# Performance work log

Measured on AMD Instinct MI355X. Metric: run time of the kernel, lower is better.

The kernel has to match this reference:

```python
import jax, jax.numpy as jnp
import numpy as np

B, L, S, V, I, H = 4096, 16, 512, 512, 512, 512  # batch, attn_length, attn_size, attn_vec_size, input_size, lstm hidden


def setup_inputs() -> dict:
    key = jax.random.key(0)
    ks = jax.random.split(key, 16)
    rn = lambda k, sh, sc=1.0: jax.random.normal(k, sh, dtype=jnp.float32) * sc
    return {
        "inputs": rn(ks[0], (B, I)),
        "cell_c": rn(ks[1], (B, H)),
        "cell_h": rn(ks[2], (B, H)),
        "attns": rn(ks[3], (B, S)),
        "attn_states": rn(ks[4], (B, L, S)),
        "W1": rn(ks[5], (I + S, I), 0.02),
        "b1": jnp.zeros((I,), jnp.float32),
        "Wx": rn(ks[6], (I, 4 * H), 0.02),
        "Wh": rn(ks[7], (H, 4 * H), 0.02),
        "b_lstm": jnp.zeros((4 * H,), jnp.float32),
        "W3": rn(ks[8], (2 * H, V), 0.02),
        "b3": jnp.zeros((V,), jnp.float32),
        "k": rn(ks[9], (1, 1, S, V), 0.02),
        "v": rn(ks[10], (1, 1, S, V), 0.02),
        "W2": rn(ks[11], (H + S, S), 0.02),
        "b2": jnp.zeros((S,), jnp.float32),
    }


def reference(inputs, cell_c, cell_h, attns, attn_states, W1, b1, Wx, Wh, b_lstm, W3, b3, k, v, W2, b2):
    # linear1: project [inputs; attns] -> cell input
    x = jnp.concatenate([inputs, attns], axis=1) @ W1 + b1  # [B, I]
    # LSTM cell step (gate order i, f, g, o)
    gates = x @ Wx + cell_h @ Wh + b_lstm  # [B, 4H]
    i, f, g, o = jnp.split(gates, 4, axis=1)
    c_new = jax.nn.sigmoid(f) * cell_c + jax.nn.sigmoid(i) * jnp.tanh(g)
    h_new = jax.nn.sigmoid(o) * jnp.tanh(c_new)
    # attention over attn_states with query = concat(new_state)
    query = jnp.concatenate([c_new, h_new], axis=1)  # [B, 2H]
    # 1x1 conv over [B, L, 1, S] with kernel [1,1,S,V] == matmul over S
    hf = jnp.einsum('bls,sv->blv', attn_states, k[0, 0])  # [B, L, V]
    y = query @ W3 + b3  # [B, V]
    t = jnp.tanh(hf + y[:, None, :])  # [B, L, V]
    # reduce_sum(v * t, [2,3]) with v [1,1,S,V] broadcast against t [B,L,1,V]
    # == einsum over V with v summed over its S axis (t independent of S axis)
    vsum = v[0, 0].sum(axis=0)  # [V]
    s = jnp.einsum('blv,v->bl', t, vsum)  # [B, L]
    a = jax.nn.softmax(s, axis=1)
    d = jnp.einsum('bl,bls->bs', a, attn_states)  # new_attns [B, S]
    # output projection on [cell_output; new_attns]
    output = jnp.concatenate([h_new, d], axis=1) @ W2 + b2  # [B, S]
    # shift attention window: drop oldest, append output
    new_attn_states = jnp.concatenate([attn_states[:, 1:, :], output[:, None, :]], axis=1)
    new_attn_states = new_attn_states.reshape(inputs.shape[0], L * S)
    return output, c_new, h_new, d, new_attn_states
```

## Files before the change

### kernel.cpp

```cpp
#include <hip/hip_runtime.h>
#include <hip/hip_bf16.h>
#include <math.h>

#define BB 4096
#define LL 16
#define SS 512
#define VV 512
#define II 512
#define HH 512

typedef __attribute__((ext_vector_type(4))) float f32x4;
typedef __attribute__((ext_vector_type(8))) short short8;

#define GLOBAL_AS __attribute__((address_space(1)))
#define LDS_AS __attribute__((address_space(3)))

__device__ __forceinline__ unsigned short f2bf(float f) {
    union { float f; unsigned u; } c; c.f = f;
    unsigned u = c.u + 0x7FFFu + ((c.u >> 16) & 1u);
    return (unsigned short)(u >> 16);
}
__device__ __forceinline__ float bf2f(unsigned short u) {
    union { unsigned u; float f; } c; c.u = ((unsigned)u) << 16;
    return c.f;
}
__device__ __forceinline__ float fast_tanh(float x) {
    return 1.f - 2.f / (__expf(2.f * x) + 1.f);
}

template<int MODE, int NF>
__global__ __launch_bounds__(256) void gemm_mfma(
    const ushort* __restrict__ A, const ushort* __restrict__ Bt,
    const float* __restrict__ bias, void* __restrict__ C, float* __restrict__ C2,
    int ldc, int M, int N, int K) {
    constexpr int BN = NF * 32;
    __shared__ ushort Als[128 * 64];
    __shared__ ushort Bls[BN * 64];
    const int tid  = threadIdx.x;
    const int lane = tid & 63;
    const int w    = tid >> 6;
    const int wm   = w >> 1, wn = w & 1;
    const int brow = blockIdx.y * 128;
    const int bcol = blockIdx.x * BN;
    f32x4 acc[4][NF] = {};
    const int nkt = K >> 6;
    for (int kt = 0; kt < nkt; ++kt) {
        __syncthreads();
        #pragma unroll
        for (int i = 0; i < 4; ++i) {
            int c0 = i * 256 + w * 64;
            int c  = c0 + lane;
            int row = c >> 3, sl = c & 7;
            const ushort* gp = A + (size_t)(brow + row) * K + kt * 64 + ((sl ^ (row & 7)) * 8);
            __builtin_amdgcn_global_load_lds((const GLOBAL_AS void*)gp,
                                             (LDS_AS void*)(Als + c0 * 8), 16, 0, 0);
        }
        #pragma unroll
        for (int i = 0; i < NF; ++i) {
            int c0 = i * 256 + w * 64;
            int c  = c0 + lane;
            int row = c >> 3, sl = c & 7;
            const ushort* gp = Bt + (size_t)(bcol + row) * K + kt * 64 + ((sl ^ (row & 7)) * 8);
            __builtin_amdgcn_global_load_lds((const GLOBAL_AS void*)gp,
                                             (LDS_AS void*)(Bls + c0 * 8), 16, 0, 0);
        }
        __syncthreads();
        const char* AlsB = (const char*)Als;
        const char* BlsB = (const char*)Bls;
        #pragma unroll
        for (int kh = 0; kh < 2; ++kh) {
            int ks = kh * 4 + (lane >> 4);
            short8 a[4], b[NF];
            #pragma unroll
            for (int m = 0; m < 4; ++m) {
                int row = wm * 64 + m * 16 + (lane & 15);
                a[m] = *(const short8*)(AlsB + (row * 8 + (ks ^ (row & 7))) * 16);
            }
            #pragma unroll
            for (int n = 0; n < NF; ++n) {
                int row = wn * (NF * 16) + n * 16 + (lane & 15);
                b[n] = *(const short8*)(BlsB + (row * 8 + (ks ^ (row & 7))) * 16);
            }
            #pragma unroll
            for (int m = 0; m < 4; ++m)
                #pragma unroll
                for (int n = 0; n < NF; ++n)
                    acc[m][n] = __builtin_amdgcn_mfma_f32_16x16x32_bf16(a[m], b[n], acc[m][n], 0, 0, 0);
        }
    }
    #pragma unroll
    for (int m = 0; m < 4; ++m)
        #pragma unroll
        for (int n = 0; n < NF; ++n)
            #pragma unroll
            for (int r = 0; r < 4; ++r) {
                int gm = brow + wm * 64 + m * 16 + (lane >> 4) * 4 + r;
                int gc = bcol + wn * (NF * 16) + n * 16 + (lane & 15);
                float v = acc[m][n][r] + bias[gc];
                if (MODE == 1) ((ushort*)C)[(size_t)gm * ldc + gc] = f2bf(v);
                else           ((float*)C)[(size_t)gm * ldc + gc] = v;
                if (MODE == 2) C2[((size_t)gm * 16 + 15) * 512 + gc] = v;
            }
}

__global__ __launch_bounds__(512, 4) void score_all(
    const float* __restrict__ ASf, const ushort* __restrict__ Bt,
    const float* __restrict__ Y, const float* __restrict__ vsum,
    float* __restrict__ o_ns, float* __restrict__ o_d, ushort* __restrict__ A7) {
    __shared__ ushort Als[64 * 64];
    __shared__ ushort Bls[512 * 64];
    __shared__ float sred[8][64];
    __shared__ float s_lds[64];
    const int tid  = threadIdx.x;
    const int lane = tid & 63;
    const int w    = tid >> 6;
    const int l15  = lane & 15, l4 = lane >> 4;
    const int brow = blockIdx.x * 64;
    const int bg0  = brow >> 4;
    f32x4 acc[4][4] = {};
    for (int kt = 0; kt < 8; ++kt) {
        __syncthreads();
        {
            int chunk = tid;
            int row = chunk >> 3, slot = chunk & 7;
            int gslot = slot ^ (row & 7);
            const float* gp = ASf + (size_t)(brow + row) * 512 + kt * 64 + gslot * 8;
            float4 f0 = *(const float4*)gp;
            float4 f1 = *(const float4*)(gp + 4);
            short8 pk;
            pk[0] = (short)f2bf(f0.x); pk[1] = (short)f2bf(f0.y);
            pk[2] = (short)f2bf(f0.z); pk[3] = (short)f2bf(f0.w);
            pk[4] = (short)f2bf(f1.x); pk[5] = (short)f2bf(f1.y);
            pk[6] = (short)f2bf(f1.z); pk[7] = (short)f2bf(f1.w);
            *(short8*)((char*)Als + chunk * 16) = pk;
        }
        #pragma unroll
        for (int i = 0; i < 8; ++i) {
            int c0 = i * 512 + w * 64;
            int c  = c0 + lane;
            int row = c >> 3, sl = c & 7;
            const ushort* gp = Bt + (size_t)row * 512 + kt * 64 + ((sl ^ (row & 7)) * 8);
            __builtin_amdgcn_global_load_lds((const GLOBAL_AS void*)gp,
                                             (LDS_AS void*)(Bls + c0 * 8), 16, 0, 0);
        }
        __syncthreads();
        const char* AlsB = (const char*)Als;
        const char* BlsB = (const char*)Bls;
        #pragma unroll
        for (int kh = 0; kh < 2; ++kh) {
            int ks = kh * 4 + l4;
            short8 a[4], b[4];
            #pragma unroll
            for (int m = 0; m < 4; ++m) {
                int row = m * 16 + l15;
                a[m] = *(const short8*)(AlsB + (row * 8 + (ks ^ (row & 7))) * 16);
            }
            #pragma unroll
            for (int n = 0; n < 4; ++n) {
                int rowb = w * 64 + n * 16 + l15;
                b[n] = *(const short8*)(BlsB + (rowb * 8 + (ks ^ (rowb & 7))) * 16);
            }
            #pragma unroll
            for (int m = 0; m < 4; ++m)
                #pragma unroll
                for (int n = 0; n < 4; ++n)
                    acc[m][n] = __builtin_amdgcn_mfma_f32_16x16x32_bf16(a[m], b[n], acc[m][n], 0, 0, 0);
        }
    }
    float part[4][4] = {};
    #pragma unroll
    for (int m = 0; m < 4; ++m) {
        int yb = bg0 + m;
        #pragma unroll
        for (int n = 0; n < 4; ++n) {
            int gc = w * 64 + n * 16 + l15;
            float yv = Y[(size_t)yb * 512 + gc];
            float vs = vsum[gc];
            #pragma unroll
            for (int r = 0; r < 4; ++r)
                part[m][r] += fast_tanh(acc[m][n][r] + yv) * vs;
        }
    }
    #pragma unroll
    for (int m = 0; m < 4; ++m)
        #pragma unroll
        for (int r = 0; r < 4; ++r) {
            float v = part[m][r];
            v += __shfl_xor(v, 1); v += __shfl_xor(v, 2);
            v += __shfl_xor(v, 4); v += __shfl_xor(v, 8);
            if (l15 == 0) sred[w][m * 16 + l4 * 4 + r] = v;
        }
    __syncthreads();
    if (tid < 64) {
        float v = 0.f;
        #pragma unroll
        for (int q = 0; q < 8; ++q) v += sred[q][tid];
        s_lds[tid] = v;
    }
    __syncthreads();

    {
        const int bat = w >> 1;
        const int bg  = bg0 + bat;
        const int c   = (w & 1) * 256 + lane * 4;
        float mx = -1e30f;
        #pragma unroll
        for (int l = 0; l < LL; ++l) mx = fmaxf(mx, s_lds[bat * 16 + l]);
        float wgt[LL]; float sum = 0.f;
        #pragma unroll
        for (int l = 0; l < LL; ++l) { wgt[l] = __expf(s_lds[bat * 16 + l] - mx); sum += wgt[l]; }
        const float inv = 1.f / sum;
        float d0 = 0.f, d1 = 0.f, d2 = 0.f, d3 = 0.f;
        #pragma unroll
        for (int l = 0; l < LL; ++l) {
            float4 v = *(const float4*)(ASf + ((size_t)bg * 16 + l) * 512 + c);
            if (l >= 1)
                *(float4*)(o_ns + ((size_t)bg * 16 + l - 1) * 512 + c) = v;
            d0 += wgt[l] * v.x; d1 += wgt[l] * v.y;
            d2 += wgt[l] * v.z; d3 += wgt[l] * v.w;
        }
        d0 *= inv; d1 *= inv; d2 *= inv; d3 *= inv;
        float4 dv; dv.x = d0; dv.y = d1; dv.z = d2; dv.w = d3;
        *(float4*)(o_d + (size_t)bg * 512 + c) = dv;
        ushort4 uv; uv.x = f2bf(d0); uv.y = f2bf(d1); uv.z = f2bf(d2); uv.w = f2bf(d3);
        *(ushort4*)(A7 + (size_t)bg * 1024 + 512 + c) = uv;
    }
}

struct TrJob { const float* srcA; const float* srcB; int K0; ushort* dst; int N; int K; };
struct TrJobs { TrJob j[5]; };

__global__ void tr_cvt_all(TrJobs jobs) {
    TrJob jb = jobs.j[blockIdx.z];
    int bn = blockIdx.x, bk = blockIdx.y;
    if (bn * 32 >= jb.N || bk * 32 >= jb.K) return;
    __shared__ float tile[32][33];
    int tx = threadIdx.x, ty = threadIdx.y;
    #pragma unroll
    for (int j = 0; j < 4; ++j) {
        int k = bk * 32 + ty + j * 8;
        const float* s = (k < jb.K0) ? (jb.srcA + (size_t)k * jb.N)
                                     : (jb.srcB + (size_t)(k - jb.K0) * jb.N);
        tile[ty + j * 8][tx] = s[bn * 32 + tx];
    }
    __syncthreads();
    #pragma unroll
    for (int j = 0; j < 4; ++j) {
        int n = bn * 32 + ty + j * 8;
        jb.dst[(size_t)n * jb.K + bk * 32 + tx] = f2bf(tile[tx][ty + j * 8]);
    }
}

struct CvJobs { const float* src[3]; ushort* dst[3]; };
__global__ void cvt_all(CvJobs jobs) {
    const float* src = jobs.src[blockIdx.y];
    ushort* dst = jobs.dst[blockIdx.y];
    int idx = blockIdx.x * 256 + threadIdx.x;
    int i4 = idx & 127, row = idx >> 7;
    float4 v = *(const float4*)(src + (size_t)row * 512 + i4 * 4);
    ushort4 o; o.x = f2bf(v.x); o.y = f2bf(v.y); o.z = f2bf(v.z); o.w = f2bf(v.w);
    *(ushort4*)(dst + (size_t)row * 1024 + i4 * 4) = o;
}

__global__ void lstm_ew(const float4* __restrict__ g4, const float4* __restrict__ cc4,
                        float4* __restrict__ c4, float4* __restrict__ h4,
                        ushort* __restrict__ A4, ushort* __restrict__ A7) {
    int idx = blockIdx.x * 256 + threadIdx.x;
    int b = idx >> 7, q = idx & 127;
    const float4* g = g4 + (size_t)b * 512;
    float4 gi = g[q], gf = g[q + 128], gg = g[q + 256], go = g[q + 384];
    float4 cc = cc4[idx];
    float4 c, h;
    #pragma unroll
    for (int j = 0; j < 4; ++j) {
        float fi = ((const float*)&gi)[j], ff = ((const float*)&gf)[j];
        float fg = ((const float*)&gg)[j], fo = ((const float*)&go)[j];
        float si = 1.f / (1.f + __expf(-fi));
        float sf = 1.f / (1.f + __expf(-ff));
        float so = 1.f / (1.f + __expf(-fo));
        float cv = sf * ((const float*)&cc)[j] + si * tanhf(fg);
        ((float*)&c)[j] = cv;
        ((float*)&h)[j] = so * tanhf(cv);
    }
    c4[idx] = c; h4[idx] = h;
    ushort4 uc, uh;
    uc.x = f2bf(c.x); uc.y = f2bf(c.y); uc.z = f2bf(c.z); uc.w = f2bf(c.w);
    uh.x = f2bf(h.x); uh.y = f2bf(h.y); uh.z = f2bf(h.z); uh.w = f2bf(h.w);
    *(ushort4*)(A4 + (size_t)b * 1024 + q * 4) = uc;
    *(ushort4*)(A4 + (size_t)b * 1024 + 512 + q * 4) = uh;
    *(ushort4*)(A7 + (size_t)b * 1024 + q * 4) = uh;
}

__global__ void vsum_k(const float* __restrict__ Vm, float* __restrict__ out) {
    __shared__ float red[8][32];
    int tc = threadIdx.x & 31, ts = threadIdx.x >> 5;
    int v = blockIdx.x * 32 + tc;
    float acc = 0.f;
    for (int s = ts; s < SS; s += 8) acc += Vm[(size_t)s * VV + v];
    red[ts][tc] = acc;
    __syncthreads();
    if (ts == 0) {
        float t = 0.f;
        #pragma unroll
        for (int j = 0; j < 8; ++j) t += red[j][tc];
        out[v] = t;
    }
}

extern "C" void kernel_launch(void* const* d_in, const int* in_sizes, int n_in,
                              void* d_out, int out_size, void* d_ws, size_t ws_size,
                              hipStream_t stream) {
    const float* inputs      = (const float*)d_in[0];
    const float* cell_c      = (const float*)d_in[1];
    const float* cell_h      = (const float*)d_in[2];
    const float* attns       = (const float*)d_in[3];
    const float* attn_states = (const float*)d_in[4];
    const float* W1          = (const float*)d_in[5];
    const float* b1          = (const float*)d_in[6];
    const float* Wx          = (const float*)d_in[7];
    const float* Wh          = (const float*)d_in[8];
    const float* b_lstm      = (const float*)d_in[9];
    const float* W3          = (const float*)d_in[10];
    const float* b3          = (const float*)d_in[11];
    const float* kmat        = (const float*)d_in[12];
    const float* vmat        = (const float*)d_in[13];
    const float* W2          = (const float*)d_in[14];
    const float* b2          = (const float*)d_in[15];

    float* o_out = (float*)d_out;
    float* o_c   = o_out + (size_t)BB * HH;
    float* o_h   = o_c   + (size_t)BB * HH;
    float* o_d   = o_h   + (size_t)BB * HH;
    float* o_ns  = o_d   + (size_t)BB * SS;

    float* ws_gates = (float*)d_ws;
    float* ws_y     = ws_gates + (size_t)BB * 4 * HH;
    float* ws_vsum  = ws_y + (size_t)BB * VV;
    ushort* A1    = (ushort*)(ws_vsum + VV);
    ushort* A2    = A1 + (size_t)BB * 1024;
    ushort* A4    = A2 + (size_t)BB * 1024;
    ushort* A7    = A4 + (size_t)BB * 1024;
    ushort* W1t   = A7 + (size_t)BB * 1024;
    ushort* WxWht = W1t + (size_t)512 * 1024;
    ushort* W3t   = WxWht + (size_t)2048 * 1024;
    ushort* W2t   = W3t + (size_t)512 * 1024;
    ushort* kTt   = W2t + (size_t)512 * 1024;

    TrJobs tj;
    tj.j[0] = {W1, W1, 1024, W1t, 512, 1024};
    tj.j[1] = {Wx, Wh, 512, WxWht, 2048, 1024};
    tj.j[2] = {W3, W3, 1024, W3t, 512, 1024};
    tj.j[3] = {W2, W2, 1024, W2t, 512, 1024};
    tj.j[4] = {kmat, kmat, 512, kTt, 512, 512};
    tr_cvt_all<<<dim3(64, 32, 5), dim3(32, 8), 0, stream>>>(tj);
    CvJobs cj;
    cj.src[0] = inputs; cj.dst[0] = A1;
    cj.src[1] = attns;  cj.dst[1] = A1 + 512;
    cj.src[2] = cell_h; cj.dst[2] = A2 + 512;
    cvt_all<<<dim3(BB * 128 / 256, 3), 256, 0, stream>>>(cj);
    vsum_k<<<16, 256, 0, stream>>>(vmat, ws_vsum);

    gemm_mfma<1, 1><<<dim3(512 / 32, BB / 128), 256, 0, stream>>>(
        A1, W1t, b1, A2, nullptr, 1024, BB, 512, 1024);
    gemm_mfma<0, 4><<<dim3(2048 / 128, BB / 128), 256, 0, stream>>>(
        A2, WxWht, b_lstm, ws_gates, nullptr, 2048, BB, 2048, 1024);
    lstm_ew<<<BB * 128 / 256, 256, 0, stream>>>(
        (const float4*)ws_gates, (const float4*)cell_c,
        (float4*)o_c, (float4*)o_h, A4, A7);
    gemm_mfma<0, 1><<<dim3(512 / 32, BB / 128), 256, 0, stream>>>(
        A4, W3t, b3, ws_y, nullptr, 512, BB, 512, 1024);
    score_all<<<BB * LL / 64, 512, 0, stream>>>(
        attn_states, kTt, ws_y, ws_vsum, o_ns, o_d, A7);
    gemm_mfma<2, 1><<<dim3(512 / 32, BB / 128), 256, 0, stream>>>(
        A7, W2t, b2, o_out, o_ns, 512, BB, 512, 1024);
}
```

Baseline: 235.4 us.

## Fuse LSTM elementwise into gate GEMM and double-buffer score_all K loop

Adds a gate GEMM whose weight columns are permuted at transpose time so each tile holds matching i/f/g/o columns. The LSTM elementwise step then runs in the GEMM epilogue, removing the fp32 gates buffer write and read and one kernel launch. Separately, score_all now streams K in 32-wide steps with double-buffered per-wave B tiles and prefetched A registers, cutting its LDS footprint and overlapping loads with MFMA. The fused epilogue writes scalar, poorly coalesced stores, and the hand-written waitcnt counts must match the number of loads in flight to stay correct.

```diff
diff --git a/kernel.cpp b/kernel.cpp
--- a/kernel.cpp
+++ b/kernel.cpp
@@ -103,12 +103,89 @@
             }
 }
 
+__global__ __launch_bounds__(256) void gemm_gates(
+    const ushort* __restrict__ A, const ushort* __restrict__ Bt,
+    const float* __restrict__ bias, const float* __restrict__ cc,
+    float* __restrict__ o_c, float* __restrict__ o_h,
+    ushort* __restrict__ A4, ushort* __restrict__ A7) {
+    __shared__ ushort Als[128 * 64];
+    __shared__ ushort Bls[64 * 64];
+    const int tid = threadIdx.x, lane = tid & 63, w = tid >> 6;
+    const int l15 = lane & 15, l4 = lane >> 4;
+    const int brow = blockIdx.y * 128;
+    const int xb = blockIdx.x;
+    f32x4 acc[2][4] = {};
+    for (int kt = 0; kt < 16; ++kt) {
+        __syncthreads();
+        #pragma unroll
+        for (int i = 0; i < 4; ++i) {
+            int c0 = i * 256 + w * 64, c = c0 + lane;
+            int row = c >> 3, sl = c & 7;
+            const ushort* gp = A + (size_t)(brow + row) * 1024 + kt * 64 + ((sl ^ (row & 7)) * 8);
+            __builtin_amdgcn_global_load_lds((const GLOBAL_AS void*)gp,
+                                             (LDS_AS void*)(Als + c0 * 8), 16, 0, 0);
+        }
+        #pragma unroll
+        for (int i = 0; i < 2; ++i) {
+            int c0 = i * 256 + w * 64, c = c0 + lane;
+            int row = c >> 3, sl = c & 7;
+            const ushort* gp = Bt + (size_t)(xb * 64 + row) * 1024 + kt * 64 + ((sl ^ (row & 7)) * 8);
+            __builtin_amdgcn_global_load_lds((const GLOBAL_AS void*)gp,
+                                             (LDS_AS void*)(Bls + c0 * 8), 16, 0, 0);
+        }
+        __syncthreads();
+        const char* AlsB = (const char*)Als;
+        const char* BlsB = (const char*)Bls;
+        #pragma unroll
+        for (int kh = 0; kh < 2; ++kh) {
+            int ks = kh * 4 + l4;
+            short8 a[2], b[4];
+            #pragma unroll
+            for (int m = 0; m < 2; ++m) {
+                int row = w * 32 + m * 16 + l15;
+                a[m] = *(const short8*)(AlsB + (row * 8 + (ks ^ (row & 7))) * 16);
+            }
+            #pragma unroll
+            for (int n = 0; n < 4; ++n) {
+                int row = n * 16 + l15;
+                b[n] = *(const short8*)(BlsB + (row * 8 + (ks ^ (row & 7))) * 16);
+            }
+            #pragma unroll
+            for (int m = 0; m < 2; ++m)
+                #pragma unroll
+                for (int n = 0; n < 4; ++n)
+                    acc[m][n] = __builtin_amdgcn_mfma_f32_16x16x32_bf16(a[m], b[n], acc[m][n], 0, 0, 0);
+        }
+    }
+    const int h = xb * 16 + l15;
+    #pragma unroll
+    for (int m = 0; m < 2; ++m)
+        #pragma unroll
+        for (int r = 0; r < 4; ++r) {
+            int gm = brow + w * 32 + m * 16 + l4 * 4 + r;
+            float gi = acc[m][0][r] + bias[h];
+            float gf = acc[m][1][r] + bias[512 + h];
+            float gg = acc[m][2][r] + bias[1024 + h];
+            float go = acc[m][3][r] + bias[1536 + h];
+            float si = 1.f / (1.f + __expf(-gi));
+            float sf = 1.f / (1.f + __expf(-gf));
+            float so = 1.f / (1.f + __expf(-go));
+            float cv = sf * cc[(size_t)gm * 512 + h] + si * tanhf(gg);
+            float hn = so * tanhf(cv);
+            o_c[(size_t)gm * 512 + h] = cv;
+            o_h[(size_t)gm * 512 + h] = hn;
+            A4[(size_t)gm * 1024 + h] = f2bf(cv);
+            A4[(size_t)gm * 1024 + 512 + h] = f2bf(hn);
+            A7[(size_t)gm * 1024 + h] = f2bf(hn);
+        }
+}
+
 __global__ __launch_bounds__(512, 4) void score_all(
     const float* __restrict__ ASf, const ushort* __restrict__ Bt,
     const float* __restrict__ Y, const float* __restrict__ vsum,
     float* __restrict__ o_ns, float* __restrict__ o_d, ushort* __restrict__ A7) {
-    __shared__ ushort Als[64 * 64];
-    __shared__ ushort Bls[512 * 64];
+    __shared__ ushort Als[64 * 40];
+    __shared__ ushort Bls[8][2][2048];
     __shared__ float sred[8][64];
     __shared__ float s_lds[64];
     const int tid  = threadIdx.x;
@@ -117,56 +194,65 @@
     const int l15  = lane & 15, l4 = lane >> 4;
     const int brow = blockIdx.x * 64;
     const int bg0  = brow >> 4;
+    const int arow = tid >> 3, aq = tid & 7;
+    const float* agp = ASf + (size_t)(brow + arow) * 512 + aq * 4;
+    const char* AlsB = (const char*)Als;
     f32x4 acc[4][4] = {};
-    for (int kt = 0; kt < 8; ++kt) {
-        __syncthreads();
+
+    #pragma unroll
+    for (int i = 0; i < 4; ++i) {
+        int cl = i * 64 + lane;
+        int r = cl >> 2, sl = cl & 3;
+        const ushort* gp = Bt + (size_t)(w * 64 + r) * 512 + ((sl ^ ((r >> 1) & 3)) * 8);
+        __builtin_amdgcn_global_load_lds((const GLOBAL_AS void*)gp,
+            (LDS_AS void*)(&Bls[w][0][i * 512] + lane * 8), 16, 0, 0);
+    }
+    float4 af = *(const float4*)agp;
+
+    #pragma unroll
+    for (int kt = 0; kt < 16; ++kt) {
+        const int buf = kt & 1;
+        asm volatile("s_waitcnt lgkmcnt(0)" ::: "memory");
+        __builtin_amdgcn_s_barrier();
         {
-            int chunk = tid;
-            int row = chunk >> 3, slot = chunk & 7;
-            int gslot = slot ^ (row & 7);
-            const float* gp = ASf + (size_t)(brow + row) * 512 + kt * 64 + gslot * 8;
-            float4 f0 = *(const float4*)gp;
-            float4 f1 = *(const float4*)(gp + 4);
-            short8 pk;
-            pk[0] = (short)f2bf(f0.x); pk[1] = (short)f2bf(f0.y);
-            pk[2] = (short)f2bf(f0.z); pk[3] = (short)f2bf(f0.w);
-            pk[4] = (short)f2bf(f1.x); pk[5] = (short)f2bf(f1.y);
-            pk[6] = (short)f2bf(f1.z); pk[7] = (short)f2bf(f1.w);
-            *(short8*)((char*)Als + chunk * 16) = pk;
-        }
-        #pragma unroll
-        for (int i = 0; i < 8; ++i) {
-            int c0 = i * 512 + w * 64;
-            int c  = c0 + lane;
-            int row = c >> 3, sl = c & 7;
-            const ushort* gp = Bt + (size_t)row * 512 + kt * 64 + ((sl ^ (row & 7)) * 8);
-            __builtin_amdgcn_global_load_lds((const GLOBAL_AS void*)gp,
-                                             (LDS_AS void*)(Bls + c0 * 8), 16, 0, 0);
-        }
-        __syncthreads();
-        const char* AlsB = (const char*)Als;
-        const char* BlsB = (const char*)Bls;
-        #pragma unroll
-        for (int kh = 0; kh < 2; ++kh) {
-            int ks = kh * 4 + l4;
-            short8 a[4], b[4];
-            #pragma unroll
-            for (int m = 0; m < 4; ++m) {
-                int row = m * 16 + l15;
-                a[m] = *(const short8*)(AlsB + (row * 8 + (ks ^ (row & 7))) * 16);
-            }
-            #pragma unroll
-            for (int n = 0; n < 4; ++n) {
-                int rowb = w * 64 + n * 16 + l15;
-                b[n] = *(const short8*)(BlsB + (rowb * 8 + (ks ^ (rowb & 7))) * 16);
-            }
-            #pragma unroll
-            for (int m = 0; m < 4; ++m)
-                #pragma unroll
-                for (int n = 0; n < 4; ++n)
-                    acc[m][n] = __builtin_amdgcn_mfma_f32_16x16x32_bf16(a[m], b[n], acc[m][n], 0, 0, 0);
-        }
-    }
+            ushort4 u; u.x = f2bf(af.x); u.y = f2bf(af.y); u.z = f2bf(af.z); u.w = f2bf(af.w);
+            *(ushort4*)((char*)Als + arow * 80 + aq * 8) = u;
+        }
+        if (kt < 15) {
+            #pragma unroll
+            for (int i = 0; i < 4; ++i) {
+                int cl = i * 64 + lane;
+                int r = cl >> 2, sl = cl & 3;
+                const ushort* gp = Bt + (size_t)(w * 64 + r) * 512 + (kt + 1) * 32
+                                   + ((sl ^ ((r >> 1) & 3)) * 8);
+                __builtin_amdgcn_global_load_lds((const GLOBAL_AS void*)gp,
+                    (LDS_AS void*)(&Bls[w][buf ^ 1][i * 512] + lane * 8), 16, 0, 0);
+            }
+            af = *(const float4*)(agp + (kt + 1) * 32);
+        }
+        asm volatile("s_waitcnt lgkmcnt(0)" ::: "memory");
+        __builtin_amdgcn_s_barrier();
+        if (kt < 15) asm volatile("s_waitcnt vmcnt(5)" ::: "memory");
+        else         asm volatile("s_waitcnt vmcnt(0)" ::: "memory");
+        short8 a[4], b[4];
+        #pragma unroll
+        for (int m = 0; m < 4; ++m) {
+            int row = m * 16 + l15;
+            a[m] = *(const short8*)(AlsB + row * 80 + l4 * 16);
+        }
+        #pragma unroll
+        for (int n = 0; n < 4; ++n) {
+            int r = n * 16 + l15;
+            int sl = l4 ^ ((r >> 1) & 3);
+            b[n] = *(const short8*)((const char*)&Bls[w][buf][0] + r * 64 + sl * 16);
+        }
+        #pragma unroll
+        for (int m = 0; m < 4; ++m)
+            #pragma unroll
+            for (int n = 0; n < 4; ++n)
+                acc[m][n] = __builtin_amdgcn_mfma_f32_16x16x32_bf16(a[m], b[n], acc[m][n], 0, 0, 0);
+    }
+
     float part[4][4] = {};
     #pragma unroll
     for (int m = 0; m < 4; ++m) {
@@ -227,7 +313,7 @@
     }
 }
 
-struct TrJob { const float* srcA; const float* srcB; int K0; ushort* dst; int N; int K; };
+struct TrJob { const float* srcA; const float* srcB; int K0; ushort* dst; int N; int K; int perm; };
 struct TrJobs { TrJob j[5]; };
 
 __global__ void tr_cvt_all(TrJobs jobs) {
@@ -247,7 +333,12 @@
     #pragma unroll
     for (int j = 0; j < 4; ++j) {
         int n = bn * 32 + ty + j * 8;
-        jb.dst[(size_t)n * jb.K + bk * 32 + tx] = f2bf(tile[tx][ty + j * 8]);
+        int nd = n;
+        if (jb.perm) {
+            int g = n >> 9, u = n & 511;
+            nd = (u >> 4) * 64 + g * 16 + (u & 15);
+        }
+        jb.dst[(size_t)nd * jb.K + bk * 32 + tx] = f2bf(tile[tx][ty + j * 8]);
     }
 }
 
@@ -260,35 +351,6 @@
     float4 v = *(const float4*)(src + (size_t)row * 512 + i4 * 4);
     ushort4 o; o.x = f2bf(v.x); o.y = f2bf(v.y); o.z = f2bf(v.z); o.w = f2bf(v.w);
     *(ushort4*)(dst + (size_t)row * 1024 + i4 * 4) = o;
-}
-
-__global__ void lstm_ew(const float4* __restrict__ g4, const float4* __restrict__ cc4,
-                        float4* __restrict__ c4, float4* __restrict__ h4,
-                        ushort* __restrict__ A4, ushort* __restrict__ A7) {
-    int idx = blockIdx.x * 256 + threadIdx.x;
-    int b = idx >> 7, q = idx & 127;
-    const float4* g = g4 + (size_t)b * 512;
-    float4 gi = g[q], gf = g[q + 128], gg = g[q + 256], go = g[q + 384];
-    float4 cc = cc4[idx];
-    float4 c, h;
-    #pragma unroll
-    for (int j = 0; j < 4; ++j) {
-        float fi = ((const float*)&gi)[j], ff = ((const float*)&gf)[j];
-        float fg = ((const float*)&gg)[j], fo = ((const float*)&go)[j];
-        float si = 1.f / (1.f + __expf(-fi));
-        float sf = 1.f / (1.f + __expf(-ff));
-        float so = 1.f / (1.f + __expf(-fo));
-        float cv = sf * ((const float*)&cc)[j] + si * tanhf(fg);
-        ((float*)&c)[j] = cv;
-        ((float*)&h)[j] = so * tanhf(cv);
-    }
-    c4[idx] = c; h4[idx] = h;
-    ushort4 uc, uh;
-    uc.x = f2bf(c.x); uc.y = f2bf(c.y); uc.z = f2bf(c.z); uc.w = f2bf(c.w);
-    uh.x = f2bf(h.x); uh.y = f2bf(h.y); uh.z = f2bf(h.z); uh.w = f2bf(h.w);
-    *(ushort4*)(A4 + (size_t)b * 1024 + q * 4) = uc;
-    *(ushort4*)(A4 + (size_t)b * 1024 + 512 + q * 4) = uh;
-    *(ushort4*)(A7 + (size_t)b * 1024 + q * 4) = uh;
 }
 
 __global__ void vsum_k(const float* __restrict__ Vm, float* __restrict__ out) {
@@ -333,25 +395,24 @@
     float* o_d   = o_h   + (size_t)BB * HH;
     float* o_ns  = o_d   + (size_t)BB * SS;
 
-    float* ws_gates = (float*)d_ws;
-    float* ws_y     = ws_gates + (size_t)BB * 4 * HH;
+    float* ws_y     = (float*)d_ws;
     float* ws_vsum  = ws_y + (size_t)BB * VV;
     ushort* A1    = (ushort*)(ws_vsum + VV);
     ushort* A2    = A1 + (size_t)BB * 1024;
     ushort* A4    = A2 + (size_t)BB * 1024;
     ushort* A7    = A4 + (size_t)BB * 1024;
     ushort* W1t   = A7 + (size_t)BB * 1024;
-    ushort* WxWht = W1t + (size_t)512 * 1024;
-    ushort* W3t   = WxWht + (size_t)2048 * 1024;
+    ushort* WBt   = W1t + (size_t)512 * 1024;
+    ushort* W3t   = WBt + (size_t)2048 * 1024;
     ushort* W2t   = W3t + (size_t)512 * 1024;
     ushort* kTt   = W2t + (size_t)512 * 1024;
 
     TrJobs tj;
-    tj.j[0] = {W1, W1, 1024, W1t, 512, 1024};
-    tj.j[1] = {Wx, Wh, 512, WxWht, 2048, 1024};
-    tj.j[2] = {W3, W3, 1024, W3t, 512, 1024};
-    tj.j[3] = {W2, W2, 1024, W2t, 512, 1024};
-    tj.j[4] = {kmat, kmat, 512, kTt, 512, 512};
+    tj.j[0] = {W1, W1, 1024, W1t, 512, 1024, 0};
+    tj.j[1] = {Wx, Wh, 512, WBt, 2048, 1024, 1};
+    tj.j[2] = {W3, W3, 1024, W3t, 512, 1024, 0};
+    tj.j[3] = {W2, W2, 1024, W2t, 512, 1024, 0};
+    tj.j[4] = {kmat, kmat, 512, kTt, 512, 512, 0};
     tr_cvt_all<<<dim3(64, 32, 5), dim3(32, 8), 0, stream>>>(tj);
     CvJobs cj;
     cj.src[0] = inputs; cj.dst[0] = A1;
@@ -362,11 +423,8 @@
 
     gemm_mfma<1, 1><<<dim3(512 / 32, BB / 128), 256, 0, stream>>>(
         A1, W1t, b1, A2, nullptr, 1024, BB, 512, 1024);
-    gemm_mfma<0, 4><<<dim3(2048 / 128, BB / 128), 256, 0, stream>>>(
-        A2, WxWht, b_lstm, ws_gates, nullptr, 2048, BB, 2048, 1024);
-    lstm_ew<<<BB * 128 / 256, 256, 0, stream>>>(
-        (const float4*)ws_gates, (const float4*)cell_c,
-        (float4*)o_c, (float4*)o_h, A4, A7);
+    gemm_gates<<<dim3(32, BB / 128), 256, 0, stream>>>(
+        A2, WBt, b_lstm, cell_c, o_c, o_h, A4, A7);
     gemm_mfma<0, 1><<<dim3(512 / 32, BB / 128), 256, 0, stream>>>(
         A4, W3t, b3, ws_y, nullptr, 512, BB, 512, 1024);
     score_all<<<BB * LL / 64, 512, 0, stream>>>(
```

New measurement: 244.5 us. 3.8% more time.
